# Kernel tuning notes

Measured on AMD Instinct MI355X. Metric: run time of the kernel, lower is better.

## Reference

```python
import jax, jax.numpy as jnp
import numpy as np

N, E = 4096, 131072
IN, HID, OUT = 128, 128, 256
H4, C4 = 4, HID            # first/middle GAT: 4 heads of 128 -> concat 512
CAT = H4 * C4              # 512
NH, DK = 8, OUT // 8       # dense MHA
EPS_LN = 1e-5


def setup_inputs() -> dict:
    key = jax.random.key(0)
    ks = jax.random.split(key, 32)
    s = 0.05
    inp = {
        "x": jax.random.normal(ks[0], (N, IN), jnp.float32),
        "edge_index": jax.random.randint(ks[1], (2, E), 0, N, jnp.int64),
        # GAT layer 0: in=128, heads=4, out=128
        "W0": jax.random.normal(ks[2], (IN, H4 * C4)) * s,
        "as0": jax.random.normal(ks[3], (H4, C4)) * s,
        "ad0": jax.random.normal(ks[4], (H4, C4)) * s,
        "b0": jnp.zeros((H4 * C4,)),
        # GAT layer 1: in=512, heads=4, out=128
        "W1": jax.random.normal(ks[5], (CAT, H4 * C4)) * s,
        "as1": jax.random.normal(ks[6], (H4, C4)) * s,
        "ad1": jax.random.normal(ks[7], (H4, C4)) * s,
        "b1": jnp.zeros((H4 * C4,)),
        # GAT layer 2: in=512, heads=1, out=256
        "W2": jax.random.normal(ks[8], (CAT, OUT)) * s,
        "as2": jax.random.normal(ks[9], (1, OUT)) * s,
        "ad2": jax.random.normal(ks[10], (1, OUT)) * s,
        "b2": jnp.zeros((OUT,)),
        # LayerNorms
        "g0": jnp.ones((CAT,)), "be0": jnp.zeros((CAT,)),
        "g1": jnp.ones((CAT,)), "be1": jnp.zeros((CAT,)),
        "g2": jnp.ones((OUT,)), "be2": jnp.zeros((OUT,)),
        # dense MHA on output_dim=256
        "wq": jax.random.normal(ks[11], (OUT, OUT)) * s, "bq": jnp.zeros((OUT,)),
        "wk": jax.random.normal(ks[12], (OUT, OUT)) * s, "bk": jnp.zeros((OUT,)),
        "wv": jax.random.normal(ks[13], (OUT, OUT)) * s, "bv": jnp.zeros((OUT,)),
        "wo": jax.random.normal(ks[14], (OUT, OUT)) * s, "bo": jnp.zeros((OUT,)),
    }
    return inp


def _layer_norm(x, g, b):
    mu = x.mean(-1, keepdims=True)
    var = ((x - mu) ** 2).mean(-1, keepdims=True)
    return (x - mu) * jax.lax.rsqrt(var + EPS_LN) * g + b


def _gat(x, src, dst, W, a_src, a_dst, bias, heads, out_c):
    # PyG GATConv (concat=True, negative_slope=0.2, self-loops pre-added)
    n = x.shape[0]
    xl = (x @ W).reshape(n, heads, out_c)            # [N,H,C]
    al_s = (xl * a_src).sum(-1)                      # [N,H]
    al_d = (xl * a_dst).sum(-1)                      # [N,H]
    alpha = jax.nn.leaky_relu(al_s[src] + al_d[dst], 0.2)  # [Etot,H]
    m = jax.ops.segment_max(alpha, dst, num_segments=n)
    e = jnp.exp(alpha - m[dst])
    denom = jax.ops.segment_sum(e, dst, num_segments=n)
    w = e / (denom[dst] + 1e-16)                     # [Etot,H]
    msg = w[:, :, None] * xl[src]                    # [Etot,H,C]
    out = jax.ops.segment_sum(msg, dst, num_segments=n)
    return out.reshape(n, heads * out_c) + bias


def _mha(x, wq, bq, wk, bk, wv, bv, wo, bo):
    # x: [1,N,D], 8 heads
    B, S, D = x.shape
    def split(y):
        return y.reshape(B, S, NH, DK).transpose(0, 2, 1, 3)
    Q, K, V = split(x @ wq + bq), split(x @ wk + bk), split(x @ wv + bv)
    scores = jnp.einsum('bhqd,bhkd->bhqk', Q, K) / np.sqrt(DK)
    attn = jax.nn.softmax(scores, axis=-1)
    out = jnp.einsum('bhqk,bhkd->bhqd', attn, V)
    out = out.transpose(0, 2, 1, 3).reshape(B, S, D)
    return out @ wo + bo


def reference(x, edge_index, W0, as0, ad0, b0, W1, as1, ad1, b1, W2, as2, ad2, b2,
              g0, be0, g1, be1, g2, be2, wq, bq, wk, bk, wv, bv, wo, bo):
    n = x.shape[0]
    loops = jnp.arange(n, dtype=edge_index.dtype)
    src = jnp.concatenate([edge_index[0], loops])
    dst = jnp.concatenate([edge_index[1], loops])

    # layer 0: in=128 -> 512; residual None (128 != 512)
    h = jax.nn.elu(_gat(x, src, dst, W0, as0, ad0, b0, H4, C4))
    h = _layer_norm(h, g0, be0)

    # layer 1: 512 -> 512; residual applies
    res = h
    h = jax.nn.elu(_gat(h, src, dst, W1, as1, ad1, b1, H4, C4))
    h = _layer_norm(h, g1, be1)
    h = h + res

    # layer 2: 512 -> 256, 1 head
    h = _gat(h, src, dst, W2, as2, ad2, b2, 1, OUT)
    h = _layer_norm(h, g2, be2)

    # dense self-attention over all nodes as one sequence
    h = _mha(h[None], wq, bq, wk, bk, wv, bv, wo, bo)[0]
    return h
```

## Files before the change

kernel.cpp:

```cpp
#include <hip/hip_runtime.h>
#include <math.h>

typedef __attribute__((ext_vector_type(8))) short short8;
typedef __attribute__((ext_vector_type(4))) float float4v;

#define QS 0.2550354f

#if __has_builtin(__builtin_amdgcn_exp2f)
#define EXP2(x) __builtin_amdgcn_exp2f(x)
#else
#define EXP2(x) __expf((x)*0.6931471805599453f)
#endif

__device__ __forceinline__ float waveReduceSum(float v){
  #pragma unroll
  for(int o=32;o>0;o>>=1) v += __shfl_down(v,o,64);
  return v;
}
__device__ __forceinline__ unsigned short f2bf(float f){
  unsigned int u = __float_as_uint(f);
  return (unsigned short)((u + 0x7FFFu + ((u>>16)&1u)) >> 16);
}
__device__ __forceinline__ float bf2f(unsigned short u){
  return __uint_as_float(((unsigned int)u)<<16);
}

__global__ __launch_bounds__(256) void prep(const float* __restrict__ x, unsigned short* __restrict__ xb,
                     const float* __restrict__ W0, unsigned short* __restrict__ W0t,
                     const float* __restrict__ W1, unsigned short* __restrict__ W1t,
                     const float* __restrict__ W2, unsigned short* __restrict__ W2t,
                     const float* __restrict__ wq, const float* __restrict__ wk,
                     const float* __restrict__ wv, unsigned short* __restrict__ wqkvt,
                     const float* __restrict__ bq, const float* __restrict__ bk,
                     const float* __restrict__ bv, float* __restrict__ bqkv,
                     const float* __restrict__ wo, unsigned short* __restrict__ wot,
                     const float* __restrict__ as0, const float* __restrict__ ad0, unsigned short* __restrict__ S0,
                     const float* __restrict__ as1, const float* __restrict__ ad1, unsigned short* __restrict__ S1,
                     const float* __restrict__ as2, const float* __restrict__ ad2, unsigned short* __restrict__ S2,
                     const int* __restrict__ ei, int E, int Etot, int* __restrict__ hist){
  int b = blockIdx.x, t = threadIdx.x;
  if(b < 256){
    int i = (b*256 + t)*8;
    float4 u0 = *(const float4*)(x + i);
    float4 u1 = *(const float4*)(x + i + 4);
    short8 o;
    o[0]=(short)f2bf(u0.x); o[1]=(short)f2bf(u0.y); o[2]=(short)f2bf(u0.z); o[3]=(short)f2bf(u0.w);
    o[4]=(short)f2bf(u1.x); o[5]=(short)f2bf(u1.y); o[6]=(short)f2bf(u1.z); o[7]=(short)f2bf(u1.w);
    *(short8*)(xb + i) = o;
    return;
  }
  if(b == 256){ bqkv[t] = bq[t]*QS; bqkv[256+t] = bk[t]; bqkv[512+t] = bv[t]; return; }
  if(b < 433){
    __shared__ unsigned short tile[64][65];
    int tb = b - 257;
    const float* src; unsigned short* dst; int K,N,roff,local; float sc = 1.f;
    if(tb<16){src=W0;dst=W0t;K=128;N=512;local=tb;roff=0;}
    else if(tb<80){src=W1;dst=W1t;K=512;N=512;local=tb-16;roff=0;}
    else if(tb<112){src=W2;dst=W2t;K=512;N=256;local=tb-80;roff=0;}
    else if(tb<128){src=wq;dst=wqkvt;K=256;N=256;local=tb-112;roff=0;sc=QS;}
    else if(tb<144){src=wk;dst=wqkvt;K=256;N=256;local=tb-128;roff=256;}
    else if(tb<160){src=wv;dst=wqkvt;K=256;N=256;local=tb-144;roff=512;}
    else {src=wo;dst=wot;K=256;N=256;local=tb-160;roff=0;}
    int ntiles = N>>6;
    int k0 = (local/ntiles)*64, n0 = (local%ntiles)*64;
    int r4 = t>>4, c4 = (t&15)*4;
    #pragma unroll
    for(int it=0;it<4;it++){
      int row = r4 + it*16;
      float4 v = *(const float4*)(src + (size_t)(k0+row)*N + n0 + c4);
      tile[row][c4+0]=f2bf(v.x*sc);
      tile[row][c4+1]=f2bf(v.y*sc);
      tile[row][c4+2]=f2bf(v.z*sc);
      tile[row][c4+3]=f2bf(v.w*sc);
    }
    __syncthreads();
    int r8 = t>>3, c8 = (t&7)*8;
    #pragma unroll
    for(int it=0;it<2;it++){
      int n = r8 + it*32;
      short8 o;
      #pragma unroll
      for(int j=0;j<8;j++) o[j] = (short)tile[c8+j][n];
      *(short8*)(dst + (size_t)(n0+n+roff)*K + k0 + c8) = o;
    }
    return;
  }
  if(b >= 1585){
    int e = (b-1585)*256 + t;
    if(e < Etot){
      int d = (e<E) ? (ei[E+e]&4095) : (e-E);
      atomicAdd(&hist[d], 1);
    }
    return;
  }
  int bb = b - 433;
  const float *W,*as,*ad; unsigned short* S; int K,C,H,k;
  if(bb<128){W=W0;as=as0;ad=ad0;S=S0;K=128;C=128;H=4;k=bb;}
  else if(bb<640){W=W1;as=as1;ad=ad1;S=S1;K=512;C=128;H=4;k=bb-128;}
  else {W=W2;as=as2;ad=ad2;S=S2;K=512;C=256;H=1;k=bb-640;}
  int D = H*C;
  __shared__ float s1[4], s2[4];
  int lane=t&63, wid=t>>6;
  for(int h=0;h<H;h++){
    float ps=0.f, pd=0.f;
    for(int c=t;c<C;c+=256){
      float wv2 = W[k*D + h*C + c];
      ps += wv2*as[h*C+c];
      pd += wv2*ad[h*C+c];
    }
    ps = waveReduceSum(ps); pd = waveReduceSum(pd);
    if(lane==0){ s1[wid]=ps; s2[wid]=pd; }
    __syncthreads();
    if(t==0){
      float u=s1[0]+s1[1]+s1[2]+s1[3], v=s2[0]+s2[1]+s2[2]+s2[3];
      S[h*K+k]=f2bf(u); S[(4+h)*K+k]=f2bf(v);
    }
    __syncthreads();
  }
  if(t==0){
    for(int h=H;h<4;h++){ S[h*K+k]=0; S[(4+h)*K+k]=0; }
    for(int r=8;r<16;r++) S[r*K+k]=0;
  }
}

__global__ __launch_bounds__(1024) void csr_scan(const int* __restrict__ hist,
                                                 int* __restrict__ rp,
                                                 int* __restrict__ wcnt, int N){
  __shared__ int sh[1024];
  int t = threadIdx.x;
  int base[4];
  int s = 0;
  #pragma unroll
  for(int i=0;i<4;i++){ base[i]=s; s += hist[t*4+i]; }
  sh[t] = s;
  __syncthreads();
  for(int off=1; off<1024; off<<=1){
    int x = (t>=off) ? sh[t-off] : 0;
    __syncthreads();
    sh[t] += x;
    __syncthreads();
  }
  int excl = (t==0) ? 0 : sh[t-1];
  #pragma unroll
  for(int i=0;i<4;i++){
    int v = excl + base[i];
    rp[t*4+i] = v; wcnt[t*4+i] = v;
  }
  if(t==1023) rp[N] = excl + s;
}

__device__ __forceinline__ void gemm_body(int bx, int by,
                          const unsigned short* __restrict__ A, const unsigned short* __restrict__ Bt,
                          const float* __restrict__ bias, float* __restrict__ C,
                          unsigned short* __restrict__ Cb, unsigned short* __restrict__ VtT,
                          const unsigned short* __restrict__ Wsd, float* __restrict__ als,
                          float* __restrict__ ald, int M, int K, int N,
                          unsigned short* As, unsigned short* Bs){
  int t = threadIdx.x, lane = t & 63, w = t >> 6;
  int m = lane & 15, g = lane >> 4;
  int bm = by * 64, bn = bx * 64;

  int sr = t >> 3;
  int sc = (t & 7) * 8;
  const unsigned short* Ap = A  + (size_t)(bm + sr)*K + sc;
  const unsigned short* Bp = Bt + (size_t)(bn + sr)*K + sc;
  bool doC = (Wsd != nullptr) && (bx == 0);

  float4v acc[4];
  #pragma unroll
  for(int nt=0;nt<4;nt++) acc[nt] = (float4v){0.f,0.f,0.f,0.f};
  float4v acc2 = (float4v){0.f,0.f,0.f,0.f};

  short8 a0 = *(const short8*)(Ap);
  short8 a1 = *(const short8*)(Ap + 32*K);
  short8 b0 = *(const short8*)(Bp);
  short8 b1 = *(const short8*)(Bp + 32*K);

  int buf = 0;
  for(int k0=0;k0<K;k0+=64){
    *(short8*)&As[buf*4608 + sr*72 + sc]      = a0;
    *(short8*)&As[buf*4608 + (sr+32)*72 + sc] = a1;
    *(short8*)&Bs[buf*4608 + sr*72 + sc]      = b0;
    *(short8*)&Bs[buf*4608 + (sr+32)*72 + sc] = b1;
    if(k0+64 < K){
      a0 = *(const short8*)(Ap + k0+64);
      a1 = *(const short8*)(Ap + 32*K + k0+64);
      b0 = *(const short8*)(Bp + k0+64);
      b1 = *(const short8*)(Bp + 32*K + k0+64);
    }
    __syncthreads();

    #pragma unroll
    for(int ks=0;ks<2;ks++){
      short8 aA = *(const short8*)&As[buf*4608 + (w*16 + m)*72 + ks*32 + g*8];
      #pragma unroll
      for(int nt=0;nt<4;nt++){
        short8 bB = *(const short8*)&Bs[buf*4608 + (nt*16 + m)*72 + ks*32 + g*8];
        acc[nt] = __builtin_amdgcn_mfma_f32_16x16x32_bf16(aA, bB, acc[nt], 0,0,0);
      }
      if(doC){
        short8 bW = *(const short8*)(Wsd + m*K + k0 + ks*32 + g*8);
        acc2 = __builtin_amdgcn_mfma_f32_16x16x32_bf16(aA, bW, acc2, 0,0,0);
      }
    }
    buf ^= 1;
  }

  if(VtT != nullptr && bn >= 512){
    __syncthreads();
    unsigned short* T = As;
    #pragma unroll
    for(int nt=0;nt<4;nt++){
      int col = bn + nt*16 + m;
      float bv = bias ? bias[col] : 0.f;
      unsigned int r0 = __float_as_uint(acc[nt][0]+bv) + 0x8000u;
      unsigned int r1 = __float_as_uint(acc[nt][1]+bv) + 0x8000u;
      unsigned int r2 = __float_as_uint(acc[nt][2]+bv) + 0x8000u;
      unsigned int r3 = __float_as_uint(acc[nt][3]+bv) + 0x8000u;
      uint2 pk;
      pk.x = __builtin_amdgcn_perm(r1, r0, 0x07060302u);
      pk.y = __builtin_amdgcn_perm(r3, r2, 0x07060302u);
      *(uint2*)&T[(nt*16 + m)*72 + w*16 + g*4] = pk;
    }
    __syncthreads();
    int d  = t >> 2;
    int qc = (t & 3) * 16;
    short8 v0 = *(const short8*)&T[d*72 + qc];
    short8 v1 = *(const short8*)&T[d*72 + qc + 8];
    unsigned short* dst = VtT + (size_t)(bn - 512 + d)*M + bm + qc;
    *(short8*)(dst)     = v0;
    *(short8*)(dst + 8) = v1;
    return;
  }

  #pragma unroll
  for(int nt=0;nt<4;nt++){
    int col = bn + nt*16 + m;
    float bv = bias ? bias[col] : 0.f;
    #pragma unroll
    for(int r=0;r<4;r++){
      int row = bm + w*16 + g*4 + r;
      float v = acc[nt][r] + bv;
      if(C)  C[(size_t)row*N + col]  = v;
      if(Cb) Cb[(size_t)row*N + col] = f2bf(v);
    }
  }
  if(doC){
    #pragma unroll
    for(int r=0;r<4;r++){
      int row = bm + w*16 + g*4 + r;
      if(m<4)      als[row*4 + m]     = acc2[r];
      else if(m<8) ald[row*4 + (m-4)] = acc2[r];
    }
  }
}

__global__ __launch_bounds__(256) void gemm_mfma(const unsigned short* __restrict__ A,
                                                 const unsigned short* __restrict__ Bt,
                                                 const float* __restrict__ bias,
                                                 float* __restrict__ C,
                                                 unsigned short* __restrict__ Cb,
                                                 unsigned short* __restrict__ VtT,
                                                 const unsigned short* __restrict__ Wsd,
                                                 float* __restrict__ als,
                                                 float* __restrict__ ald,
                                                 int M, int K, int N){
  __shared__ unsigned short As[2*4608];
  __shared__ unsigned short Bs[2*4608];
  gemm_body(blockIdx.x, blockIdx.y, A, Bt, bias, C, Cb, VtT, Wsd, als, ald, M, K, N, As, Bs);
}

__global__ __launch_bounds__(256) void gemm0_scatter(const unsigned short* __restrict__ A,
                                                     const unsigned short* __restrict__ Bt,
                                                     unsigned short* __restrict__ Cb,
                                                     const unsigned short* __restrict__ Wsd,
                                                     float* __restrict__ als, float* __restrict__ ald,
                                                     const int* __restrict__ ei, int E, int Etot,
                                                     int* __restrict__ wcnt, int* __restrict__ col){
  __shared__ unsigned short As[2*4608];
  __shared__ unsigned short Bs[2*4608];
  int u = blockIdx.x;
  if(u < 512){
    gemm_body(u & 7, u >> 3, A, Bt, nullptr, nullptr, Cb, nullptr, Wsd, als, ald, 4096, 128, 512, As, Bs);
  } else {
    int e = (u-512)*256 + threadIdx.x;
    if(e < Etot){
      int s,d;
      if(e < E){ s = ei[e]&4095; d = ei[E+e]&4095; } else { s = d = e - E; }
      int pos = atomicAdd(&wcnt[d], 1);
      col[pos] = s;
    }
  }
}

#define CE 128
__global__ void gat_gather_ln(const int* __restrict__ rp,
                              const int* __restrict__ col,
                              const unsigned short* __restrict__ xlb,
                              const float* __restrict__ als,
                              const float* __restrict__ ald,
                              const float* __restrict__ bias,
                              const float* __restrict__ gw,
                              const float* __restrict__ be,
                              const float* __restrict__ res,
                              float* __restrict__ out,
                              unsigned short* __restrict__ outb,
                              int D, int logC, int do_elu){
  int n = blockIdx.x, t = threadIdx.x;
  int c0 = t*2;
  int h = c0 >> logC;
  int rowW = D >> 1;
  float4 advv = *(const float4*)(ald + n*4);
  int start = rp[n], end = rp[n+1];
  const unsigned int* xw = (const unsigned int*)xlb;

  __shared__ float pw[2][CE*4];
  __shared__ int offs[2][CE];

  float acc0=0.f, acc1=0.f, den=0.f;
  int nch = (end - start + CE - 1) / CE;

  {
    int cnt = min(CE, end-start);
    if(t < cnt){
      int s = col[start+t];
      offs[0][t] = s*rowW;
      float4 av = *(const float4*)(als + s*4);
      #pragma unroll
      for(int hh=0;hh<4;hh++){
        float a = ((const float*)&av)[hh] + ((const float*)&advv)[hh];
        a = a>0.f ? a : 0.2f*a;
        pw[0][t*4+hh] = __expf(a);
      }
    }
  }

  for(int c=0;c<nch;c++){
    __syncthreads();
    if(c+1 < nch){
      int base = start + (c+1)*CE;
      int cnt = min(CE, end-base);
      int b2 = (c+1)&1;
      if(t < cnt){
        int s = col[base+t];
        offs[b2][t] = s*rowW;
        float4 av = *(const float4*)(als + s*4);
        #pragma unroll
        for(int hh=0;hh<4;hh++){
          float a = ((const float*)&av)[hh] + ((const float*)&advv)[hh];
          a = a>0.f ? a : 0.2f*a;
          pw[b2][t*4+hh] = __expf(a);
        }
      }
    }
    int base = start + c*CE;
    int cnt = min(CE, end-base);
    int b = c&1;
    #pragma unroll 8
    for(int j=0;j<cnt;j++){
      float p = pw[b][j*4+h];
      unsigned int u = xw[offs[b][j] + t];
      acc0 += p * bf2f((unsigned short)(u & 0xffffu));
      acc1 += p * bf2f((unsigned short)(u >> 16));
      den += p;
    }
  }

  float inv_d = 1.f/(den + 1e-16f);
  float v0 = acc0*inv_d + bias[c0];
  float v1 = acc1*inv_d + bias[c0+1];
  if(do_elu){
    v0 = v0>0.f ? v0 : expm1f(v0);
    v1 = v1>0.f ? v1 : expm1f(v1);
  }
  __shared__ float sh[4];
  int lane=t&63, wid=t>>6, nw = blockDim.x>>6;
  float sum = waveReduceSum(v0+v1);
  if(lane==0) sh[wid]=sum;
  __syncthreads();
  float mean = 0.f;
  for(int i=0;i<nw;i++) mean += sh[i];
  mean /= (float)D;
  __syncthreads();
  float d0 = v0-mean, d1 = v1-mean;
  float vs = waveReduceSum(d0*d0 + d1*d1);
  if(lane==0) sh[wid]=vs;
  __syncthreads();
  float var = 0.f;
  for(int i=0;i<nw;i++) var += sh[i];
  var /= (float)D;
  float inv = rsqrtf(var + 1e-5f);
  float y0 = d0*inv*gw[c0]   + be[c0];
  float y1 = d1*inv*gw[c0+1] + be[c0+1];
  if(res){ float2 rv = *(const float2*)(res + n*D + c0); y0 += rv.x; y1 += rv.y; }
  if(out) *(float2*)(out + n*D + c0) = make_float2(y0, y1);
  if(outb) ((unsigned int*)outb)[n*rowW + t] =
      (unsigned int)f2bf(y0) | ((unsigned int)f2bf(y1) << 16);
}

#define KS 2
__global__ __launch_bounds__(256) void attention12(const unsigned short* __restrict__ QKV,
                                                   const unsigned short* __restrict__ Vt,
                                                   float* __restrict__ Op,
                                                   float* __restrict__ lp, int S){
  const int RS = 768;
  int qb = blockIdx.x * 64;
  int h  = blockIdx.y;
  int ks = blockIdx.z;
  int t  = threadIdx.x;
  int lane = t & 63, w = t >> 6;
  int m = lane & 15, g = lane >> 4;
  int m7 = m & 7;

  __shared__ unsigned short Ps[64*64];
  __shared__ unsigned short Vs[32*64];
  __shared__ unsigned short Ks[64*36];

  short8 aQ = *(const short8*)(QKV + (qb + w*16 + m)*RS + h*32 + g*8);

  float4v o0 = {0.f,0.f,0.f,0.f}, o1 = {0.f,0.f,0.f,0.f};
  float den = 0.f;

  int r8 = t>>3, c8 = t&7;
  int kr = t>>2, kc = (t&3)*8;
  int kA = ks*(S/KS), kB = kA + S/KS;

  short8 v  = *(const short8*)(Vt + (h*32 + r8)*S + kA + c8*8);
  short8 kv = *(const short8*)(QKV + (kA + kr)*RS + 256 + h*32 + kc);

  for(int kt=kA; kt<kB; kt+=64){
    __syncthreads();
    *(short8*)&Vs[r8*64 + ((c8 ^ (r8&7))<<3)] = v;
    *(short8*)&Ks[kr*36 + kc] = kv;
    if(kt+64 < kB){
      v  = *(const short8*)(Vt + (h*32 + r8)*S + kt+64 + c8*8);
      kv = *(const short8*)(QKV + (kt+64 + kr)*RS + 256 + h*32 + kc);
    }
    __syncthreads();

    #pragma unroll
    for(int nt=0;nt<4;nt++){
      short8 aK = *(const short8*)&Ks[(nt*16 + m)*36 + g*8];
      float4v acc = {0.f,0.f,0.f,0.f};
      acc = __builtin_amdgcn_mfma_f32_16x16x32_bf16(aK, aQ, acc, 0,0,0);
      float p0 = EXP2(acc[0]);
      float p1 = EXP2(acc[1]);
      float p2 = EXP2(acc[2]);
      float p3 = EXP2(acc[3]);
      den += (p0+p1)+(p2+p3);
      unsigned int r0 = __float_as_uint(p0) + 0x8000u;
      unsigned int r1 = __float_as_uint(p1) + 0x8000u;
      unsigned int r2 = __float_as_uint(p2) + 0x8000u;
      unsigned int r3 = __float_as_uint(p3) + 0x8000u;
      uint2 pk;
      pk.x = __builtin_amdgcn_perm(r1, r0, 0x07060302u);
      pk.y = __builtin_amdgcn_perm(r3, r2, 0x07060302u);
      *(uint2*)&Ps[(w*16 + m)*64 + (((2*nt + (g>>1)) ^ m7)<<3) + ((g&1)<<2)] = pk;
    }

    #pragma unroll
    for(int kh=0;kh<2;kh++){
      int swz = ((kh*4 + g) ^ m7) << 3;
      short8 aP  = *(const short8*)&Ps[(w*16 + m)*64 + swz];
      short8 bV0 = *(const short8*)&Vs[m*64       + swz];
      short8 bV1 = *(const short8*)&Vs[(16+m)*64  + swz];
      o0 = __builtin_amdgcn_mfma_f32_16x16x32_bf16(aP, bV0, o0, 0,0,0);
      o1 = __builtin_amdgcn_mfma_f32_16x16x32_bf16(aP, bV1, o1, 0,0,0);
    }
  }

  den += __shfl_xor(den, 16, 64);
  den += __shfl_xor(den, 32, 64);

  float* Ob = Op + (size_t)ks*S*256;
  #pragma unroll
  for(int r=0;r<4;r++){
    int q = qb + w*16 + g*4 + r;
    Ob[q*256 + h*32 + m]      = o0[r];
    Ob[q*256 + h*32 + 16 + m] = o1[r];
  }
  if(g==0){
    int q = qb + w*16 + m;
    lp[ks*S*8 + q*8 + h] = den;
  }
}

__global__ __launch_bounds__(256) void combine(const float* __restrict__ Op,
                                               const float* __restrict__ lp,
                                               unsigned short* __restrict__ aob, int S){
  int q = blockIdx.x, t = threadIdx.x;
  int h = t >> 5;
  float o = 0.f, l = 0.f;
  #pragma unroll
  for(int s=0;s<KS;s++) o += Op[(size_t)s*S*256 + q*256 + t];
  #pragma unroll
  for(int s=0;s<KS;s++) l += lp[s*S*8 + q*8 + h];
  aob[q*256 + t] = f2bf(o / l);
}

extern "C" void kernel_launch(void* const* d_in, const int* in_sizes, int n_in,
                              void* d_out, int out_size, void* d_ws, size_t ws_size,
                              hipStream_t stream) {
  const float* x   = (const float*)d_in[0];
  const int*   ei  = (const int*)d_in[1];
  const float* W0  = (const float*)d_in[2];
  const float* as0 = (const float*)d_in[3];
  const float* ad0 = (const float*)d_in[4];
  const float* b0  = (const float*)d_in[5];
  const float* W1  = (const float*)d_in[6];
  const float* as1 = (const float*)d_in[7];
  const float* ad1 = (const float*)d_in[8];
  const float* b1  = (const float*)d_in[9];
  const float* W2  = (const float*)d_in[10];
  const float* as2 = (const float*)d_in[11];
  const float* ad2 = (const float*)d_in[12];
  const float* b2  = (const float*)d_in[13];
  const float* g0  = (const float*)d_in[14];
  const float* be0 = (const float*)d_in[15];
  const float* g1  = (const float*)d_in[16];
  const float* be1 = (const float*)d_in[17];
  const float* g2  = (const float*)d_in[18];
  const float* be2 = (const float*)d_in[19];
  const float* wq  = (const float*)d_in[20];
  const float* bq  = (const float*)d_in[21];
  const float* wk  = (const float*)d_in[22];
  const float* bk  = (const float*)d_in[23];
  const float* wv  = (const float*)d_in[24];
  const float* bv  = (const float*)d_in[25];
  const float* wo  = (const float*)d_in[26];
  const float* bo  = (const float*)d_in[27];
  float* out = (float*)d_out;

  const int N = 4096;
  const int E = in_sizes[1] / 2;
  const int Etot = E + N;

  char* p = (char*)d_ws;
  auto alloc = [&](size_t bytes){ char* r = p; p += (bytes + 255) & ~(size_t)255; return r; };

  float* h0   = (float*)alloc(N*512*4);
  float* als  = (float*)alloc(N*4*4);
  float* ald  = (float*)alloc(N*4*4);
  unsigned short* xb   = (unsigned short*)alloc(N*128*2);
  unsigned short* xlb  = (unsigned short*)alloc(N*512*2);
  unsigned short* h0b  = (unsigned short*)alloc(N*512*2);
  unsigned short* h1b  = (unsigned short*)alloc(N*512*2);
  unsigned short* h2b  = (unsigned short*)alloc(N*256*2);
  unsigned short* QKVb = (unsigned short*)alloc((size_t)N*768*2);
  unsigned short* Vt   = (unsigned short*)alloc(256*N*2);
  unsigned short* aob  = (unsigned short*)alloc(N*256*2);
  unsigned short* W0t  = (unsigned short*)alloc(512*128*2);
  unsigned short* W1t  = (unsigned short*)alloc(512*512*2);
  unsigned short* W2t  = (unsigned short*)alloc(256*512*2);
  unsigned short* wqkvt= (unsigned short*)alloc(768*256*2);
  float* bqkv = (float*)alloc(768*4);
  unsigned short* wot  = (unsigned short*)alloc(256*256*2);
  unsigned short* Wsd0 = (unsigned short*)alloc(16*128*2);
  unsigned short* Wsd1 = (unsigned short*)alloc(16*512*2);
  unsigned short* Wsd2 = (unsigned short*)alloc(16*512*2);
  float* Op = (float*)alloc((size_t)KS*N*256*4);
  float* lp = (float*)alloc((size_t)KS*N*8*4);
  int* hist = (int*)alloc(N*4);
  int* wcnt = (int*)alloc(N*4);
  int* rp   = (int*)alloc((N+2)*4);
  int* col  = (int*)alloc(Etot*4);

  hipMemsetAsync(hist, 0, N*sizeof(int), stream);
  prep<<<1585 + (Etot+255)/256, 256, 0, stream>>>(x, xb, W0, W0t, W1, W1t, W2, W2t,
                                 wq, wk, wv, wqkvt, bq, bk, bv, bqkv, wo, wot,
                                 as0, ad0, Wsd0, as1, ad1, Wsd1, as2, ad2, Wsd2,
                                 ei, E, Etot, hist);

  csr_scan<<<1, 1024, 0, stream>>>(hist, rp, wcnt, N);

  gemm0_scatter<<<512 + (Etot+255)/256, 256, 0, stream>>>(xb, W0t, xlb, Wsd0, als, ald,
                                                          ei, E, Etot, wcnt, col);
  gat_gather_ln<<<N, 256, 0, stream>>>(rp, col, xlb, als, ald, b0, g0, be0,
                                       nullptr, h0, h0b, 512, 7, 1);

  gemm_mfma<<<dim3(8, 64), 256, 0, stream>>>(h0b, W1t, nullptr, nullptr, xlb, nullptr, Wsd1, als, ald, N, 512, 512);
  gat_gather_ln<<<N, 256, 0, stream>>>(rp, col, xlb, als, ald, b1, g1, be1,
                                       h0, nullptr, h1b, 512, 7, 1);

  gemm_mfma<<<dim3(4, 64), 256, 0, stream>>>(h1b, W2t, nullptr, nullptr, xlb, nullptr, Wsd2, als, ald, N, 512, 256);
  gat_gather_ln<<<N, 128, 0, stream>>>(rp, col, xlb, als, ald, b2, g2, be2,
                                       nullptr, nullptr, h2b, 256, 8, 0);

  gemm_mfma<<<dim3(12, 64), 256, 0, stream>>>(h2b, wqkvt, bqkv, nullptr, QKVb, Vt, nullptr, nullptr, nullptr, N, 256, 768);
  attention12<<<dim3(N/64, 8, KS), 256, 0, stream>>>(QKVb, Vt, Op, lp, N);
  combine<<<N, 256, 0, stream>>>(Op, lp, aob, N);
  gemm_mfma<<<dim3(4, 64), 256, 0, stream>>>(aob, wot, bo, out, nullptr, nullptr, nullptr, nullptr, nullptr, N, 256, 256);
}
```

Baseline: 263.4 us.

## Fuse split-K attention combine via last-block atomic counter and MFMA row sums

Removes the separate combine kernel. Each attention block increments a per-(query tile, head) counter, and the last of the KS split blocks merges both partial outputs and denominators and writes bf16 output. The softmax denominator is now computed with an extra MFMA against a vector of bf16 ones, which uses the same bf16-rounded probabilities as the PV product. The manual round-and-permute packing is replaced by v_cvt_pk_bf16_f32. This saves a launch and a pass over the partial buffers, at the cost of a threadfence and an atomic per block plus one extra MFMA per k-step.

```diff
diff --git a/kernel.cpp b/kernel.cpp
--- a/kernel.cpp
+++ b/kernel.cpp
@@ -37,7 +37,8 @@
                      const float* __restrict__ as0, const float* __restrict__ ad0, unsigned short* __restrict__ S0,
                      const float* __restrict__ as1, const float* __restrict__ ad1, unsigned short* __restrict__ S1,
                      const float* __restrict__ as2, const float* __restrict__ ad2, unsigned short* __restrict__ S2,
-                     const int* __restrict__ ei, int E, int Etot, int* __restrict__ hist){
+                     const int* __restrict__ ei, int E, int Etot, int* __restrict__ hist,
+                     int* __restrict__ acnt){
   int b = blockIdx.x, t = threadIdx.x;
   if(b < 256){
     int i = (b*256 + t)*8;
@@ -49,7 +50,11 @@
     *(short8*)(xb + i) = o;
     return;
   }
-  if(b == 256){ bqkv[t] = bq[t]*QS; bqkv[256+t] = bk[t]; bqkv[512+t] = bv[t]; return; }
+  if(b == 256){
+    bqkv[t] = bq[t]*QS; bqkv[256+t] = bk[t]; bqkv[512+t] = bv[t];
+    acnt[t] = 0; acnt[256+t] = 0;
+    return;
+  }
   if(b < 433){
     __shared__ unsigned short tile[64][65];
     int tb = b - 257;
@@ -402,7 +407,9 @@
 __global__ __launch_bounds__(256) void attention12(const unsigned short* __restrict__ QKV,
                                                    const unsigned short* __restrict__ Vt,
                                                    float* __restrict__ Op,
-                                                   float* __restrict__ lp, int S){
+                                                   float* __restrict__ lp,
+                                                   int* __restrict__ acnt,
+                                                   unsigned short* __restrict__ aob, int S){
   const int RS = 768;
   int qb = blockIdx.x * 64;
   int h  = blockIdx.y;
@@ -415,11 +422,15 @@
   __shared__ unsigned short Ps[64*64];
   __shared__ unsigned short Vs[32*64];
   __shared__ unsigned short Ks[64*36];
+  __shared__ int lastFlag;
 
   short8 aQ = *(const short8*)(QKV + (qb + w*16 + m)*RS + h*32 + g*8);
+  short8 vones;
+  #pragma unroll
+  for(int j=0;j<8;j++) vones[j] = (short)0x3F80;
 
   float4v o0 = {0.f,0.f,0.f,0.f}, o1 = {0.f,0.f,0.f,0.f};
-  float den = 0.f;
+  float4v lacc = {0.f,0.f,0.f,0.f};
 
   int r8 = t>>3, c8 = t&7;
   int kr = t>>2, kc = (t&3)*8;
@@ -447,14 +458,9 @@
       float p1 = EXP2(acc[1]);
       float p2 = EXP2(acc[2]);
       float p3 = EXP2(acc[3]);
-      den += (p0+p1)+(p2+p3);
-      unsigned int r0 = __float_as_uint(p0) + 0x8000u;
-      unsigned int r1 = __float_as_uint(p1) + 0x8000u;
-      unsigned int r2 = __float_as_uint(p2) + 0x8000u;
-      unsigned int r3 = __float_as_uint(p3) + 0x8000u;
       uint2 pk;
-      pk.x = __builtin_amdgcn_perm(r1, r0, 0x07060302u);
-      pk.y = __builtin_amdgcn_perm(r3, r2, 0x07060302u);
+      asm("v_cvt_pk_bf16_f32 %0, %1, %2" : "=v"(pk.x) : "v"(p0), "v"(p1));
+      asm("v_cvt_pk_bf16_f32 %0, %1, %2" : "=v"(pk.y) : "v"(p2), "v"(p3));
       *(uint2*)&Ps[(w*16 + m)*64 + (((2*nt + (g>>1)) ^ m7)<<3) + ((g&1)<<2)] = pk;
     }
 
@@ -466,11 +472,9 @@
       short8 bV1 = *(const short8*)&Vs[(16+m)*64  + swz];
       o0 = __builtin_amdgcn_mfma_f32_16x16x32_bf16(aP, bV0, o0, 0,0,0);
       o1 = __builtin_amdgcn_mfma_f32_16x16x32_bf16(aP, bV1, o1, 0,0,0);
-    }
-  }
-
-  den += __shfl_xor(den, 16, 64);
-  den += __shfl_xor(den, 32, 64);
+      lacc = __builtin_amdgcn_mfma_f32_16x16x32_bf16(aP, vones, lacc, 0,0,0);
+    }
+  }
 
   float* Ob = Op + (size_t)ks*S*256;
   #pragma unroll
@@ -479,23 +483,38 @@
     Ob[q*256 + h*32 + m]      = o0[r];
     Ob[q*256 + h*32 + 16 + m] = o1[r];
   }
-  if(g==0){
-    int q = qb + w*16 + m;
-    lp[ks*S*8 + q*8 + h] = den;
-  }
-}
-
-__global__ __launch_bounds__(256) void combine(const float* __restrict__ Op,
-                                               const float* __restrict__ lp,
-                                               unsigned short* __restrict__ aob, int S){
-  int q = blockIdx.x, t = threadIdx.x;
-  int h = t >> 5;
-  float o = 0.f, l = 0.f;
-  #pragma unroll
-  for(int s=0;s<KS;s++) o += Op[(size_t)s*S*256 + q*256 + t];
-  #pragma unroll
-  for(int s=0;s<KS;s++) l += lp[s*S*8 + q*8 + h];
-  aob[q*256 + t] = f2bf(o / l);
+  if(m==0){
+    #pragma unroll
+    for(int r=0;r<4;r++){
+      int q = qb + w*16 + g*4 + r;
+      lp[ks*S*8 + q*8 + h] = lacc[r];
+    }
+  }
+
+  __threadfence();
+  if(t==0) lastFlag = (atomicAdd(&acnt[blockIdx.x*8 + h], 1) == KS-1) ? 1 : 0;
+  __syncthreads();
+  if(lastFlag){
+    __threadfence();
+    int q  = qb + (t >> 2);
+    int c0 = h*32 + (t & 3)*8;
+    float4 s0 = *(const float4*)(Op + (size_t)q*256 + c0);
+    float4 s1 = *(const float4*)(Op + (size_t)q*256 + c0 + 4);
+    float4 u0 = *(const float4*)(Op + (size_t)S*256 + (size_t)q*256 + c0);
+    float4 u1 = *(const float4*)(Op + (size_t)S*256 + (size_t)q*256 + c0 + 4);
+    float l = lp[q*8 + h] + lp[S*8 + q*8 + h];
+    float inv = 1.f / l;
+    short8 ov;
+    ov[0] = (short)f2bf((s0.x+u0.x)*inv);
+    ov[1] = (short)f2bf((s0.y+u0.y)*inv);
+    ov[2] = (short)f2bf((s0.z+u0.z)*inv);
+    ov[3] = (short)f2bf((s0.w+u0.w)*inv);
+    ov[4] = (short)f2bf((s1.x+u1.x)*inv);
+    ov[5] = (short)f2bf((s1.y+u1.y)*inv);
+    ov[6] = (short)f2bf((s1.z+u1.z)*inv);
+    ov[7] = (short)f2bf((s1.w+u1.w)*inv);
+    *(short8*)(aob + (size_t)q*256 + c0) = ov;
+  }
 }
 
 extern "C" void kernel_launch(void* const* d_in, const int* in_sizes, int n_in,
@@ -564,12 +583,13 @@
   int* wcnt = (int*)alloc(N*4);
   int* rp   = (int*)alloc((N+2)*4);
   int* col  = (int*)alloc(Etot*4);
+  int* acnt = (int*)alloc(512*4);
 
   hipMemsetAsync(hist, 0, N*sizeof(int), stream);
   prep<<<1585 + (Etot+255)/256, 256, 0, stream>>>(x, xb, W0, W0t, W1, W1t, W2, W2t,
                                  wq, wk, wv, wqkvt, bq, bk, bv, bqkv, wo, wot,
                                  as0, ad0, Wsd0, as1, ad1, Wsd1, as2, ad2, Wsd2,
-                                 ei, E, Etot, hist);
+                                 ei, E, Etot, hist, acnt);
 
   csr_scan<<<1, 1024, 0, stream>>>(hist, rp, wcnt, N);
 
@@ -587,7 +607,6 @@
                                        nullptr, nullptr, h2b, 256, 8, 0);
 
   gemm_mfma<<<dim3(12, 64), 256, 0, stream>>>(h2b, wqkvt, bqkv, nullptr, QKVb, Vt, nullptr, nullptr, nullptr, N, 256, 768);
-  attention12<<<dim3(N/64, 8, KS), 256, 0, stream>>>(QKVb, Vt, Op, lp, N);
-  combine<<<N, 256, 0, stream>>>(Op, lp, aob, N);
+  attention12<<<dim3(N/64, 8, KS), 256, 0, stream>>>(QKVb, Vt, Op, lp, acnt, aob, N);
   gemm_mfma<<<dim3(4, 64), 256, 0, stream>>>(aob, wot, bo, out, nullptr, nullptr, nullptr, nullptr, nullptr, N, 256, 256);
 }
```

Measured after the change: 406.9 us. 54.5% more time.
